# Kernel tuning notes

Measured on AMD Instinct MI355X. Metric: run time of the kernel, lower is better.

Reference implementation:

```python
import jax, jax.numpy as jnp
import numpy as np

PH = PW = 33   # patch size of base_net
IMH = IMW = 24 # output map size (one base_net eval per pixel)
SLOPE = 0.01   # LeakyReLU negative slope used in base AnomalyNet


def _conv(x, w, b):
    y = jax.lax.conv_general_dilated(x, w, (1, 1), 'VALID',
                                     dimension_numbers=('NCHW', 'OIHW', 'NCHW'))
    return y + b[None, :, None, None]


def _pool2(x):
    return jax.lax.reduce_window(x, -jnp.inf, jax.lax.max,
                                 (1, 1, 2, 2), (1, 1, 2, 2), 'VALID')


def _base_net(p, c1w, c1b, c2w, c2b, c3w, c3b, c4w, c4b, c5w, c5b, dw, db):
    lr = lambda h: jax.nn.leaky_relu(h, SLOPE)
    h = _pool2(lr(_conv(p, c1w, c1b)))   # (N,128,14,14)
    h = _pool2(lr(_conv(h, c2w, c2b)))   # (N,128,5,5)
    h = lr(_conv(h, c3w, c3b))           # (N,128,1,1)
    h = lr(_conv(h, c4w, c4b))           # (N,256,1,1)
    h = lr(_conv(h, c5w, c5b))           # (N,128,1,1)
    h = h.reshape(h.shape[0], -1)        # (N,128)
    return h @ dw.T + db                 # (N,512)


def setup_inputs() -> dict:
    key = jax.random.key(0)
    ks = jax.random.split(key, 8)
    he = lambda k, shape, fan_in: (jax.random.normal(k, shape, jnp.float32)
                                   * np.float32(np.sqrt(2.0 / fan_in)))
    z = lambda n: jnp.zeros((n,), jnp.float32)
    return {
        'x':   jax.random.normal(ks[0], (1, 3, IMH, IMW), jnp.float32),
        'c1w': he(ks[1], (128, 3, 5, 5), 3 * 25),   'c1b': z(128),
        'c2w': he(ks[2], (128, 128, 5, 5), 128 * 25), 'c2b': z(128),
        'c3w': he(ks[3], (128, 128, 5, 5), 128 * 25), 'c3b': z(128),
        'c4w': he(ks[4], (256, 128, 1, 1), 128),      'c4b': z(256),
        'c5w': he(ks[5], (128, 256, 1, 1), 256),      'c5b': z(128),
        'dw':  he(ks[6], (512, 128), 128),            'db': z(512),
    }


def reference(x, c1w, c1b, c2w, c2b, c3w, c3b, c4w, c4b, c5w, c5b, dw, db):
    B, C = x.shape[0], x.shape[1]
    pady, padx = PH - 1, PW - 1
    # multiPoolPrepare: zero-pad so every output pixel has a full PHxPW patch
    xp = jnp.pad(x, ((0, 0), (0, 0),
                     (pady // 2, pady - pady // 2),
                     (padx // 2, padx - padx // 2)))
    # all overlapping PHxPW patches, one per output pixel (replaces the i,j loops)
    patches = jax.lax.conv_general_dilated_patches(
        xp, (PH, PW), (1, 1), 'VALID',
        dimension_numbers=('NCHW', 'OIHW', 'NCHW'))  # (B, C*PH*PW, IMH, IMW)
    patches = patches.reshape(B, C, PH, PW, IMH, IMW)
    patches = patches.transpose(0, 4, 5, 1, 2, 3).reshape(B * IMH * IMW, C, PH, PW)
    feats = _base_net(patches, c1w, c1b, c2w, c2b, c3w, c3b,
                      c4w, c4b, c5w, c5b, dw, db)      # (B*IMH*IMW, 512)
    return feats.reshape(B, IMH, IMW, -1).transpose(0, 3, 1, 2)  # (B,512,IMH,IMW)
```

## Files before the change

kernel.cpp:

```cpp
#include <hip/hip_runtime.h>

#define SLOPE 0.01f

typedef __attribute__((ext_vector_type(8))) short short8;
typedef __attribute__((ext_vector_type(4))) float f32x4;

__device__ __forceinline__ float lrelu(float v) { return v >= 0.f ? v : SLOPE * v; }

__device__ __forceinline__ unsigned short f2bf(float f) {
    union { float f; unsigned int u; } v; v.f = f;
    unsigned int r = v.u + 0x7fffu + ((v.u >> 16) & 1u);
    return (unsigned short)(r >> 16);
}
__device__ __forceinline__ float bf2f(unsigned short h) {
    union { unsigned int u; float f; } v; v.u = ((unsigned int)h) << 16;
    return v.f;
}
__device__ __forceinline__ unsigned short bfmax4(unsigned short a, unsigned short b,
                                                 unsigned short c, unsigned short d) {
    float m = fmaxf(fmaxf(bf2f(a), bf2f(b)), fmaxf(bf2f(c), bf2f(d)));
    union { float f; unsigned int u; } v; v.f = m;
    return (unsigned short)(v.u >> 16);
}

__device__ __forceinline__ int swz(int oc, int k, int Kdiv32) {
    return (((oc >> 4) * Kdiv32 + (k >> 5)) * 64 + ((k >> 3) & 3) * 16 + (oc & 15)) * 8 + (k & 7);
}


__global__ __launch_bounds__(256) void k_front(const float* __restrict__ x,
                                               const float* __restrict__ c1w,
                                               const float* __restrict__ c1b,
                                               const float* __restrict__ c2w,
                                               const float* __restrict__ c3w,
                                               const float* __restrict__ c4w,
                                               const float* __restrict__ c5w,
                                               const float* __restrict__ dw,
                                               unsigned short* __restrict__ P2,
                                               unsigned short* __restrict__ W2s,
                                               unsigned short* __restrict__ W3s,
                                               unsigned short* __restrict__ C4Bs,
                                               unsigned short* __restrict__ C5Bs,
                                               unsigned short* __restrict__ DWBs) {
    __shared__ float smem[9600];
    int bid = blockIdx.x, tid = threadIdx.x;

    if (bid < 1250) {
        for (int idx = tid; idx < 9600; idx += 256) smem[idx] = c1w[idx];
        __syncthreads();

        int t = bid * 256 + tid;
        int ic = t & 127;
        int rest = t >> 7;
        int B = rest % 25;
        int A = (rest / 25) % 25;
        int ph = rest / 625;
        int py = ph >> 1, px = ph & 1;
        int r0 = 2 * A + py, s0 = 2 * B + px;

        float a00 = 0.f, a01 = 0.f, a10 = 0.f, a11 = 0.f;
        const float* lw = smem + ic * 75;
        for (int c = 0; c < 3; ++c) {
            const float* xc = x + c * 576;
            const float* lwc = lw + c * 25;
#pragma unroll
            for (int ky = 0; ky < 5; ++ky) {
                int iy = r0 + ky - 16;
                bool v0 = (iy >= 0) && (iy < 24);
                bool v1 = (iy + 1 >= 0) && (iy + 1 < 24);
                if (!v0 && !v1) continue;
#pragma unroll
                for (int kx = 0; kx < 5; ++kx) {
                    int ix = s0 + kx - 16;
                    float w = lwc[ky * 5 + kx];
                    bool u0 = (ix >= 0) && (ix < 24);
                    bool u1 = (ix + 1 >= 0) && (ix + 1 < 24);
                    float x00 = (v0 && u0) ? xc[iy * 24 + ix] : 0.f;
                    float x01 = (v0 && u1) ? xc[iy * 24 + ix + 1] : 0.f;
                    float x10 = (v1 && u0) ? xc[(iy + 1) * 24 + ix] : 0.f;
                    float x11 = (v1 && u1) ? xc[(iy + 1) * 24 + ix + 1] : 0.f;
                    a00 += x00 * w; a01 += x01 * w; a10 += x10 * w; a11 += x11 * w;
                }
            }
        }
        float mx = fmaxf(fmaxf(a00, a01), fmaxf(a10, a11));
        P2[t] = f2bf(lrelu(c1b[ic] + mx));
    } else if (bid < 1506) {
        int wbid = bid - 1250;
        int oc = wbid & 127;
        const float* src = (wbid < 128) ? (c2w + oc * 3200) : (c3w + oc * 3200);
        unsigned short* dst = (wbid < 128) ? W2s : W3s;
        for (int idx = tid; idx < 3200; idx += 256) smem[idx] = src[idx];
        __syncthreads();
        for (int idx = tid; idx < 3200; idx += 256) {
            int ic = idx & 127, kpos = idx >> 7;
            dst[swz(oc, kpos * 128 + ic, 100)] = f2bf(smem[ic * 25 + kpos]);
        }
    } else {
        int e = (bid - 1506) * 256 + tid;
        if (e < 32768) {
            int oc = e >> 7, k = e & 127;
            C4Bs[swz(oc, k, 4)] = f2bf(c4w[e]);
        } else if (e < 65536) {
            int e2 = e - 32768;
            int oc = e2 >> 8, k = e2 & 255;
            C5Bs[swz(oc, k, 8)] = f2bf(c5w[e2]);
        } else {
            int e2 = e - 65536;
            int oc = e2 >> 7, k = e2 & 127;
            DWBs[swz(oc, k, 4)] = f2bf(dw[e2]);
        }
    }
}

__global__ __launch_bounds__(256) void k_conv2(const unsigned short* __restrict__ P2,
                                               const unsigned short* __restrict__ W2s,
                                               const float* __restrict__ bias,
                                               unsigned short* __restrict__ Z2) {
    int bid = blockIdx.x;
    int ph = bid / 42;
    int rem = bid % 42;
    int A = rem >> 1;
    int oh = rem & 1;
    int tid = threadIdx.x, lane = tid & 63, wid = tid >> 6;
    int m = lane & 15, bq = lane >> 4;
    int oc0 = oh * 64 + wid * 16;
    int t = oh * 4 + wid;
    const unsigned short* wbase = W2s + (t * 100 * 64 + lane) * 8;
    const unsigned short* pbase = P2 + ((ph * 25 + A) * 25) * 128 + 8 * bq;
    f32x4 acc0 = {0.f, 0.f, 0.f, 0.f}, acc1 = {0.f, 0.f, 0.f, 0.f};
    for (int kpos = 0; kpos < 25; ++kpos) {
        int ky = kpos / 5, kx = kpos % 5;
        const unsigned short* wp = wbase + kpos * 4 * 512;
        const unsigned short* p0 = pbase + (ky * 25 + m + kx) * 128;
        const unsigned short* p1 = p0 + 5 * 128;
#pragma unroll
        for (int cc = 0; cc < 4; ++cc) {
            short8 a  = *(const short8*)(wp + cc * 512);
            short8 b0 = *(const short8*)(p0 + cc * 32);
            short8 b1 = *(const short8*)(p1 + cc * 32);
            acc0 = __builtin_amdgcn_mfma_f32_16x16x32_bf16(a, b0, acc0, 0, 0, 0);
            acc1 = __builtin_amdgcn_mfma_f32_16x16x32_bf16(a, b1, acc1, 0, 0, 0);
        }
    }
    int ocb = oc0 + 4 * bq;
    float b0v = bias[ocb], b1v = bias[ocb + 1], b2v = bias[ocb + 2], b3v = bias[ocb + 3];
    unsigned short* zrow = Z2 + ((ph * 21 + A) * 21) * 128 + ocb;
    {
        ushort4 pk;
        pk.x = f2bf(lrelu(acc0.x + b0v));
        pk.y = f2bf(lrelu(acc0.y + b1v));
        pk.z = f2bf(lrelu(acc0.z + b2v));
        pk.w = f2bf(lrelu(acc0.w + b3v));
        *(ushort4*)(zrow + m * 128) = pk;
    }
    if (m >= 11) {
        ushort4 pk;
        pk.x = f2bf(lrelu(acc1.x + b0v));
        pk.y = f2bf(lrelu(acc1.y + b1v));
        pk.z = f2bf(lrelu(acc1.z + b2v));
        pk.w = f2bf(lrelu(acc1.w + b3v));
        *(ushort4*)(zrow + (m + 5) * 128) = pk;
    }
}

#define QSTR 3208
__global__ __launch_bounds__(512) void k_tail(const unsigned short* __restrict__ Z2,
                                              const unsigned short* __restrict__ W3s,
                                              const float* __restrict__ c3b,
                                              const unsigned short* __restrict__ C4Bs,
                                              const float* __restrict__ c4b,
                                              const unsigned short* __restrict__ C5Bs,
                                              const float* __restrict__ c5b,
                                              const unsigned short* __restrict__ DWBs,
                                              const float* __restrict__ db,
                                              float* __restrict__ out) {
    __shared__ unsigned short lds[59904];
    unsigned short* Qw   = lds;
    unsigned short* h3bf = lds + 16 * QSTR;
    unsigned short* h4bf = h3bf + 16 * 136;
    unsigned short* h5bf = h4bf + 16 * 264;

    int bid = blockIdx.x, tid = threadIdx.x;
    int n0 = bid * 16;
    int lane = tid & 63, w = tid >> 6;
    int m = lane & 15, bq = lane >> 4;

    for (int v = tid; v < 6400; v += 512) {
        int p = v / 400;
        int rem = v - p * 400;
        int kpos = rem >> 4;
        int ic0 = (rem & 15) * 8;
        int e = kpos / 5, f = kpos % 5;
        int n = n0 + p, i = n / 24, j = n % 24;
        int ph1 = (i & 1) * 2 + (j & 1);
        int C = (i >> 2) + e, D = (j >> 2) + f;
        int r0 = 2 * C + ((i >> 1) & 1), s0 = 2 * D + ((j >> 1) & 1);
        const unsigned short* z = Z2 + ((ph1 * 21 + r0) * 21 + s0) * 128 + ic0;
        ushort4 za0 = *(const ushort4*)(z);
        ushort4 za1 = *(const ushort4*)(z + 4);
        ushort4 zb0 = *(const ushort4*)(z + 128);
        ushort4 zb1 = *(const ushort4*)(z + 132);
        ushort4 zc0 = *(const ushort4*)(z + 21 * 128);
        ushort4 zc1 = *(const ushort4*)(z + 21 * 128 + 4);
        ushort4 zd0 = *(const ushort4*)(z + 22 * 128);
        ushort4 zd1 = *(const ushort4*)(z + 22 * 128 + 4);
        ushort4 r0v, r1v;
        r0v.x = bfmax4(za0.x, zb0.x, zc0.x, zd0.x);
        r0v.y = bfmax4(za0.y, zb0.y, zc0.y, zd0.y);
        r0v.z = bfmax4(za0.z, zb0.z, zc0.z, zd0.z);
        r0v.w = bfmax4(za0.w, zb0.w, zc0.w, zd0.w);
        r1v.x = bfmax4(za1.x, zb1.x, zc1.x, zd1.x);
        r1v.y = bfmax4(za1.y, zb1.y, zc1.y, zd1.y);
        r1v.z = bfmax4(za1.z, zb1.z, zc1.z, zd1.z);
        r1v.w = bfmax4(za1.w, zb1.w, zc1.w, zd1.w);
        unsigned short* dst = Qw + p * QSTR + rem * 8;
        *(ushort4*)(dst) = r0v;
        *(ushort4*)(dst + 4) = r1v;
    }
    __syncthreads();

    {
        const unsigned short* qb = Qw + m * QSTR + 8 * bq;
        const unsigned short* wbase = W3s + (w * 6400 + lane) * 8;
        f32x4 acc = {0.f, 0.f, 0.f, 0.f};
        for (int kpos = 0; kpos < 25; ++kpos) {
            const unsigned short* qp = qb + kpos * 128;
            const unsigned short* wp = wbase + kpos * 2048;
#pragma unroll
            for (int cc = 0; cc < 4; ++cc) {
                short8 a = *(const short8*)(wp + cc * 512);
                short8 b = *(const short8*)(qp + cc * 32);
                acc = __builtin_amdgcn_mfma_f32_16x16x32_bf16(a, b, acc, 0, 0, 0);
            }
        }
        int oc = w * 16 + bq * 4;
        uint2 pk;
        pk.x = (unsigned)f2bf(lrelu(acc.x + c3b[oc])) | ((unsigned)f2bf(lrelu(acc.y + c3b[oc + 1])) << 16);
        pk.y = (unsigned)f2bf(lrelu(acc.z + c3b[oc + 2])) | ((unsigned)f2bf(lrelu(acc.w + c3b[oc + 3])) << 16);
        *(uint2*)(&h3bf[m * 136 + oc]) = pk;
    }
    __syncthreads();

    {
        f32x4 acc[2] = {{0,0,0,0},{0,0,0,0}};
#pragma unroll
        for (int t = 0; t < 2; ++t) {
            const unsigned short* abase = C4Bs + ((w * 2 + t) * 4 * 64 + lane) * 8;
#pragma unroll
            for (int cc = 0; cc < 4; ++cc) {
                short8 a = *(const short8*)(abase + cc * 512);
                short8 b = *(const short8*)(&h3bf[m * 136 + cc * 32 + 8 * bq]);
                acc[t] = __builtin_amdgcn_mfma_f32_16x16x32_bf16(a, b, acc[t], 0, 0, 0);
            }
        }
#pragma unroll
        for (int t = 0; t < 2; ++t) {
            int oc = (w * 2 + t) * 16 + bq * 4;
            uint2 pk;
            pk.x = (unsigned)f2bf(lrelu(acc[t].x + c4b[oc])) | ((unsigned)f2bf(lrelu(acc[t].y + c4b[oc + 1])) << 16);
            pk.y = (unsigned)f2bf(lrelu(acc[t].z + c4b[oc + 2])) | ((unsigned)f2bf(lrelu(acc[t].w + c4b[oc + 3])) << 16);
            *(uint2*)(&h4bf[m * 264 + oc]) = pk;
        }
    }
    __syncthreads();

    {
        const unsigned short* abase = C5Bs + (w * 8 * 64 + lane) * 8;
        f32x4 acc = {0.f, 0.f, 0.f, 0.f};
#pragma unroll
        for (int cc = 0; cc < 8; ++cc) {
            short8 a = *(const short8*)(abase + cc * 512);
            short8 b = *(const short8*)(&h4bf[m * 264 + cc * 32 + 8 * bq]);
            acc = __builtin_amdgcn_mfma_f32_16x16x32_bf16(a, b, acc, 0, 0, 0);
        }
        int oc = w * 16 + bq * 4;
        uint2 pk;
        pk.x = (unsigned)f2bf(lrelu(acc.x + c5b[oc])) | ((unsigned)f2bf(lrelu(acc.y + c5b[oc + 1])) << 16);
        pk.y = (unsigned)f2bf(lrelu(acc.z + c5b[oc + 2])) | ((unsigned)f2bf(lrelu(acc.w + c5b[oc + 3])) << 16);
        *(uint2*)(&h5bf[m * 136 + oc]) = pk;
    }
    __syncthreads();

    {
        f32x4 acc[4] = {{0,0,0,0},{0,0,0,0},{0,0,0,0},{0,0,0,0}};
#pragma unroll
        for (int t = 0; t < 4; ++t) {
            const unsigned short* abase = DWBs + ((w * 4 + t) * 4 * 64 + lane) * 8;
#pragma unroll
            for (int cc = 0; cc < 4; ++cc) {
                short8 a = *(const short8*)(abase + cc * 512);
                short8 b = *(const short8*)(&h5bf[m * 136 + cc * 32 + 8 * bq]);
                acc[t] = __builtin_amdgcn_mfma_f32_16x16x32_bf16(a, b, acc[t], 0, 0, 0);
            }
        }
#pragma unroll
        for (int t = 0; t < 4; ++t) {
            int oc = (w * 4 + t) * 16 + bq * 4;
            out[(oc + 0) * 576 + n0 + m] = acc[t].x + db[oc + 0];
            out[(oc + 1) * 576 + n0 + m] = acc[t].y + db[oc + 1];
            out[(oc + 2) * 576 + n0 + m] = acc[t].z + db[oc + 2];
            out[(oc + 3) * 576 + n0 + m] = acc[t].w + db[oc + 3];
        }
    }
}

extern "C" void kernel_launch(void* const* d_in, const int* in_sizes, int n_in,
                              void* d_out, int out_size, void* d_ws, size_t ws_size,
                              hipStream_t stream) {
    const float* x   = (const float*)d_in[0];
    const float* c1w = (const float*)d_in[1];
    const float* c1b = (const float*)d_in[2];
    const float* c2w = (const float*)d_in[3];
    const float* c2b = (const float*)d_in[4];
    const float* c3w = (const float*)d_in[5];
    const float* c3b = (const float*)d_in[6];
    const float* c4w = (const float*)d_in[7];
    const float* c4b = (const float*)d_in[8];
    const float* c5w = (const float*)d_in[9];
    const float* c5b = (const float*)d_in[10];
    const float* dw  = (const float*)d_in[11];
    const float* db  = (const float*)d_in[12];
    float* out = (float*)d_out;

    float* ws = (float*)d_ws;
    unsigned short* P2   = (unsigned short*)(ws);
    unsigned short* Z2   = (unsigned short*)(ws + 160000);
    unsigned short* W2s  = (unsigned short*)(ws + 272896);
    unsigned short* W3s  = (unsigned short*)(ws + 477696);
    unsigned short* C4Bs = (unsigned short*)(ws + 682496);
    unsigned short* C5Bs = (unsigned short*)(ws + 698880);
    unsigned short* DWBs = (unsigned short*)(ws + 715264);

    k_front<<<2018, 256, 0, stream>>>(x, c1w, c1b, c2w, c3w, c4w, c5w, dw,
                                      P2, W2s, W3s, C4Bs, C5Bs, DWBs);
    k_conv2<<<168, 256, 0, stream>>>(P2, W2s, c2b, Z2);
    k_tail<<<36, 512, 0, stream>>>(Z2, W3s, c3b, C4Bs, c4b, C5Bs, c5b, DWBs, db, out);
}
```

Baseline: 66.97 us.

## Merge front work into uniform blocks, pack bf16 stores, regroup conv2 waves

k_front drops its three block roles and runs 256 uniform blocks of 512 threads. Each block computes 625 packed pairs of conv1 channels, rearranges one conv2/conv3 weight row, and converts a slice of the 1x1/dense weights, using 32-bit and 64-bit packed bf16 stores. k_conv2 now launches 84 blocks of 512 threads, mapping each wave to one (phase, row, oc-tile) tuple. The aim is fewer launched blocks, fewer small stores and less redundant c1w staging into shared memory. The cost is more work per thread in conv1 and fewer, larger blocks, which may lower parallelism on a GPU with many CUs.

Result: slower. 107.5 us (+60.5%).

```diff
diff --git a/kernel.cpp b/kernel.cpp
--- a/kernel.cpp
+++ b/kernel.cpp
@@ -22,13 +22,18 @@
     union { float f; unsigned int u; } v; v.f = m;
     return (unsigned short)(v.u >> 16);
 }
+__device__ __forceinline__ unsigned long long pk4(unsigned short a, unsigned short b,
+                                                  unsigned short c, unsigned short d) {
+    return (unsigned long long)a | ((unsigned long long)b << 16)
+         | ((unsigned long long)c << 32) | ((unsigned long long)d << 48);
+}
 
 __device__ __forceinline__ int swz(int oc, int k, int Kdiv32) {
     return (((oc >> 4) * Kdiv32 + (k >> 5)) * 64 + ((k >> 3) & 3) * 16 + (oc & 15)) * 8 + (k & 7);
 }
 
 
-__global__ __launch_bounds__(256) void k_front(const float* __restrict__ x,
+__global__ __launch_bounds__(512) void k_front(const float* __restrict__ x,
                                                const float* __restrict__ c1w,
                                                const float* __restrict__ c1b,
                                                const float* __restrict__ c2w,
@@ -36,102 +41,118 @@
                                                const float* __restrict__ c4w,
                                                const float* __restrict__ c5w,
                                                const float* __restrict__ dw,
-                                               unsigned short* __restrict__ P2,
+                                               unsigned* __restrict__ P2u,
                                                unsigned short* __restrict__ W2s,
                                                unsigned short* __restrict__ W3s,
                                                unsigned short* __restrict__ C4Bs,
                                                unsigned short* __restrict__ C5Bs,
                                                unsigned short* __restrict__ DWBs) {
     __shared__ float smem[9600];
-    int bid = blockIdx.x, tid = threadIdx.x;
-
-    if (bid < 1250) {
-        for (int idx = tid; idx < 9600; idx += 256) smem[idx] = c1w[idx];
-        __syncthreads();
-
-        int t = bid * 256 + tid;
-        int ic = t & 127;
-        int rest = t >> 7;
+    const int tid = threadIdx.x;
+    const int bid = blockIdx.x;
+
+    for (int idx = tid; idx < 9600; idx += 512) smem[idx] = c1w[idx];
+    __syncthreads();
+    for (int q = tid; q < 625; q += 512) {
+        int t32 = bid * 625 + q;
+        int icp = t32 & 63;
+        int rest = t32 >> 6;
         int B = rest % 25;
         int A = (rest / 25) % 25;
         int ph = rest / 625;
         int py = ph >> 1, px = ph & 1;
         int r0 = 2 * A + py, s0 = 2 * B + px;
-
-        float a00 = 0.f, a01 = 0.f, a10 = 0.f, a11 = 0.f;
-        const float* lw = smem + ic * 75;
-        for (int c = 0; c < 3; ++c) {
-            const float* xc = x + c * 576;
-            const float* lwc = lw + c * 25;
-#pragma unroll
-            for (int ky = 0; ky < 5; ++ky) {
-                int iy = r0 + ky - 16;
-                bool v0 = (iy >= 0) && (iy < 24);
-                bool v1 = (iy + 1 >= 0) && (iy + 1 < 24);
-                if (!v0 && !v1) continue;
-#pragma unroll
-                for (int kx = 0; kx < 5; ++kx) {
-                    int ix = s0 + kx - 16;
-                    float w = lwc[ky * 5 + kx];
-                    bool u0 = (ix >= 0) && (ix < 24);
-                    bool u1 = (ix + 1 >= 0) && (ix + 1 < 24);
-                    float x00 = (v0 && u0) ? xc[iy * 24 + ix] : 0.f;
-                    float x01 = (v0 && u1) ? xc[iy * 24 + ix + 1] : 0.f;
-                    float x10 = (v1 && u0) ? xc[(iy + 1) * 24 + ix] : 0.f;
-                    float x11 = (v1 && u1) ? xc[(iy + 1) * 24 + ix + 1] : 0.f;
-                    a00 += x00 * w; a01 += x01 * w; a10 += x10 * w; a11 += x11 * w;
+        unsigned packed = 0;
+#pragma unroll
+        for (int ii = 0; ii < 2; ++ii) {
+            int ic = icp * 2 + ii;
+            float a00 = 0.f, a01 = 0.f, a10 = 0.f, a11 = 0.f;
+            const float* lw = smem + ic * 75;
+            for (int c = 0; c < 3; ++c) {
+                const float* xc = x + c * 576;
+                const float* lwc = lw + c * 25;
+#pragma unroll
+                for (int ky = 0; ky < 5; ++ky) {
+                    int iy = r0 + ky - 16;
+                    bool v0 = (iy >= 0) && (iy < 24);
+                    bool v1 = (iy + 1 >= 0) && (iy + 1 < 24);
+                    if (!v0 && !v1) continue;
+#pragma unroll
+                    for (int kx = 0; kx < 5; ++kx) {
+                        int ix = s0 + kx - 16;
+                        float w = lwc[ky * 5 + kx];
+                        bool u0 = (ix >= 0) && (ix < 24);
+                        bool u1 = (ix + 1 >= 0) && (ix + 1 < 24);
+                        float x00 = (v0 && u0) ? xc[iy * 24 + ix] : 0.f;
+                        float x01 = (v0 && u1) ? xc[iy * 24 + ix + 1] : 0.f;
+                        float x10 = (v1 && u0) ? xc[(iy + 1) * 24 + ix] : 0.f;
+                        float x11 = (v1 && u1) ? xc[(iy + 1) * 24 + ix + 1] : 0.f;
+                        a00 += x00 * w; a01 += x01 * w; a10 += x10 * w; a11 += x11 * w;
+                    }
                 }
             }
-        }
-        float mx = fmaxf(fmaxf(a00, a01), fmaxf(a10, a11));
-        P2[t] = f2bf(lrelu(c1b[ic] + mx));
-    } else if (bid < 1506) {
-        int wbid = bid - 1250;
-        int oc = wbid & 127;
-        const float* src = (wbid < 128) ? (c2w + oc * 3200) : (c3w + oc * 3200);
-        unsigned short* dst = (wbid < 128) ? W2s : W3s;
-        for (int idx = tid; idx < 3200; idx += 256) smem[idx] = src[idx];
+            float mx = fmaxf(fmaxf(a00, a01), fmaxf(a10, a11));
+            unsigned short r = f2bf(lrelu(c1b[ic] + mx));
+            packed |= ((unsigned)r) << (16 * ii);
+        }
+        P2u[t32] = packed;
+    }
+
+    {
+        int oc = bid & 127;
+        const float* src = (bid < 128) ? (c2w + oc * 3200) : (c3w + oc * 3200);
+        unsigned short* dst = (bid < 128) ? W2s : W3s;
         __syncthreads();
-        for (int idx = tid; idx < 3200; idx += 256) {
-            int ic = idx & 127, kpos = idx >> 7;
-            dst[swz(oc, kpos * 128 + ic, 100)] = f2bf(smem[ic * 25 + kpos]);
-        }
-    } else {
-        int e = (bid - 1506) * 256 + tid;
-        if (e < 32768) {
-            int oc = e >> 7, k = e & 127;
-            C4Bs[swz(oc, k, 4)] = f2bf(c4w[e]);
-        } else if (e < 65536) {
-            int e2 = e - 32768;
+        for (int idx = tid; idx < 3200; idx += 512) smem[idx] = src[idx];
+        __syncthreads();
+        for (int g = tid; g < 800; g += 512) {
+            int ic0 = (g & 31) * 4;
+            int kpos = g >> 5;
+            unsigned long long v = pk4(f2bf(smem[(ic0 + 0) * 25 + kpos]),
+                                       f2bf(smem[(ic0 + 1) * 25 + kpos]),
+                                       f2bf(smem[(ic0 + 2) * 25 + kpos]),
+                                       f2bf(smem[(ic0 + 3) * 25 + kpos]));
+            *(unsigned long long*)(dst + swz(oc, kpos * 128 + ic0, 100)) = v;
+        }
+    }
+
+    if (tid < 128) {
+        int e0 = (bid * 128 + tid) * 4;
+        if (e0 < 32768) {
+            int oc = e0 >> 7, k = e0 & 127;
+            *(unsigned long long*)(C4Bs + swz(oc, k, 4)) =
+                pk4(f2bf(c4w[e0]), f2bf(c4w[e0 + 1]), f2bf(c4w[e0 + 2]), f2bf(c4w[e0 + 3]));
+        } else if (e0 < 65536) {
+            int e2 = e0 - 32768;
             int oc = e2 >> 8, k = e2 & 255;
-            C5Bs[swz(oc, k, 8)] = f2bf(c5w[e2]);
+            *(unsigned long long*)(C5Bs + swz(oc, k, 8)) =
+                pk4(f2bf(c5w[e2]), f2bf(c5w[e2 + 1]), f2bf(c5w[e2 + 2]), f2bf(c5w[e2 + 3]));
         } else {
-            int e2 = e - 65536;
+            int e2 = e0 - 65536;
             int oc = e2 >> 7, k = e2 & 127;
-            DWBs[swz(oc, k, 4)] = f2bf(dw[e2]);
-        }
-    }
-}
-
-__global__ __launch_bounds__(256) void k_conv2(const unsigned short* __restrict__ P2,
+            *(unsigned long long*)(DWBs + swz(oc, k, 4)) =
+                pk4(f2bf(dw[e2]), f2bf(dw[e2 + 1]), f2bf(dw[e2 + 2]), f2bf(dw[e2 + 3]));
+        }
+    }
+}
+
+__global__ __launch_bounds__(512) void k_conv2(const unsigned short* __restrict__ P2,
                                                const unsigned short* __restrict__ W2s,
                                                const float* __restrict__ bias,
                                                unsigned short* __restrict__ Z2) {
-    int bid = blockIdx.x;
-    int ph = bid / 42;
-    int rem = bid % 42;
-    int A = rem >> 1;
-    int oh = rem & 1;
     int tid = threadIdx.x, lane = tid & 63, wid = tid >> 6;
+    int gw = blockIdx.x * 8 + wid;
+    int ph = gw / 168;
+    int rem = gw % 168;
+    int A = rem / 8;
+    int t = rem % 8;
     int m = lane & 15, bq = lane >> 4;
-    int oc0 = oh * 64 + wid * 16;
-    int t = oh * 4 + wid;
-    const unsigned short* wbase = W2s + (t * 100 * 64 + lane) * 8;
+    const unsigned short* wbase = W2s + (t * 6400 + lane) * 8;
     const unsigned short* pbase = P2 + ((ph * 25 + A) * 25) * 128 + 8 * bq;
     f32x4 acc0 = {0.f, 0.f, 0.f, 0.f}, acc1 = {0.f, 0.f, 0.f, 0.f};
     for (int kpos = 0; kpos < 25; ++kpos) {
         int ky = kpos / 5, kx = kpos % 5;
-        const unsigned short* wp = wbase + kpos * 4 * 512;
+        const unsigned short* wp = wbase + kpos * 2048;
         const unsigned short* p0 = pbase + (ky * 25 + m + kx) * 128;
         const unsigned short* p1 = p0 + 5 * 128;
 #pragma unroll
@@ -143,7 +164,7 @@
             acc1 = __builtin_amdgcn_mfma_f32_16x16x32_bf16(a, b1, acc1, 0, 0, 0);
         }
     }
-    int ocb = oc0 + 4 * bq;
+    int ocb = t * 16 + 4 * bq;
     float b0v = bias[ocb], b1v = bias[ocb + 1], b2v = bias[ocb + 2], b3v = bias[ocb + 3];
     unsigned short* zrow = Z2 + ((ph * 21 + A) * 21) * 128 + ocb;
     {
@@ -324,6 +345,7 @@
     float* out = (float*)d_out;
 
     float* ws = (float*)d_ws;
+    unsigned*       P2u  = (unsigned*)(ws);
     unsigned short* P2   = (unsigned short*)(ws);
     unsigned short* Z2   = (unsigned short*)(ws + 160000);
     unsigned short* W2s  = (unsigned short*)(ws + 272896);
@@ -332,8 +354,8 @@
     unsigned short* C5Bs = (unsigned short*)(ws + 698880);
     unsigned short* DWBs = (unsigned short*)(ws + 715264);
 
-    k_front<<<2018, 256, 0, stream>>>(x, c1w, c1b, c2w, c3w, c4w, c5w, dw,
-                                      P2, W2s, W3s, C4Bs, C5Bs, DWBs);
-    k_conv2<<<168, 256, 0, stream>>>(P2, W2s, c2b, Z2);
+    k_front<<<256, 512, 0, stream>>>(x, c1w, c1b, c2w, c3w, c4w, c5w, dw,
+                                     P2u, W2s, W3s, C4Bs, C5Bs, DWBs);
+    k_conv2<<<84, 512, 0, stream>>>(P2, W2s, c2b, Z2);
     k_tail<<<36, 512, 0, stream>>>(Z2, W3s, c3b, C4Bs, c4b, C5Bs, c5b, DWBs, db, out);
 }
```
